# Kernel optimization log

Hardware: AMD Instinct MI355X
Metric: run time of the kernel (lower is better)

Reference implementation:

```python
import jax, jax.numpy as jnp
import numpy as np

BL = 5
N = 2 ** BL  # 32; LUT is (N+1) x (N+1)


def setup_inputs() -> dict:
    key = jax.random.key(0)
    k1, k2, k3 = jax.random.split(key, 3)
    M, K, O = 512, 256, 256
    x = jax.random.uniform(k1, (M, K), dtype=jnp.float32)              # activations in [0,1)
    W = jax.random.uniform(k2, (O, K), dtype=jnp.float32) * 2.0 - 1.0  # weights in [-1,1)
    b = jax.random.uniform(k3, (O,), dtype=jnp.float32) * 2.0 - 1.0
    # Stochastic-computing multiplication LUT: A[i, j] ~ i*j/N (floored), i,j in [0, N]
    i = np.arange(N + 1, dtype=np.float32)
    lut = jnp.asarray(np.floor(np.outer(i, i) / N), dtype=jnp.float32)
    return {"x": x, "W": W, "b": b, "lut": lut}


def _sanitize(t):
    t = jnp.where(jnp.isnan(t), jnp.zeros_like(t), t)
    return jnp.where(jnp.isinf(t), jnp.ones_like(t), t)


def sc_mat_mac_p(a, b, c, lut, n):
    # Faithful port of SC_MAT_MAC_p: quantize -> LUT gather over all (row, out) pairs ->
    # sign-correct -> reduce over K -> requantize -> add quantized bias -> rescale.
    a = _sanitize(a)
    b = _sanitize(b)
    c = _sanitize(c)
    amax = jnp.abs(a).max()
    amax = jnp.where(amax == 0, jnp.ones_like(amax), amax)
    dmax = jnp.maximum(jnp.abs(b).max(), jnp.abs(c).max())
    dmax = jnp.where(dmax == 0, jnp.ones_like(dmax), dmax)
    # SBL2 = int(log2(int(N / amax))); SN2 = 2**SBL2 (truncations match torch int())
    sn2 = 2.0 ** jnp.floor(jnp.log2(jnp.floor(n / amax)))
    sn1 = 2.0 ** jnp.floor(jnp.log2(jnp.floor(n / dmax)))
    aa = (a * sn2).astype(jnp.int32)  # [M, K], |aa| <= N
    bb = (b * sn1).astype(jnp.int32)  # [O, K], |bb| <= N
    cc = (c * sn1).astype(jnp.int32)  # [O]
    # LUT gather over the full cross product (original materializes this via
    # repeat_interleave/repeat; here it is a broadcasted gather of shape [M, O, K]).
    prod = lut[jnp.abs(aa)[:, None, :], jnp.abs(bb)[None, :, :]]          # [M, O, K]
    sgn = (jnp.sign(aa)[:, None, :] * jnp.sign(bb)[None, :, :]).astype(prod.dtype)
    x9 = (sgn * prod).sum(axis=-1)                                        # [M, O]
    d = (x9 / sn2).astype(jnp.int32) + cc[None, :]
    return d.astype(jnp.float32) / sn1


def reference(x, W, b, lut):
    # out = linear(x); out.data = SC_MAT_MAC_p(...)  -> value is the SC result,
    # gradient path is the dense linear (straight-through via .data assignment).
    lin = x @ W.T + b
    p = sc_mat_mac_p(x, W, b, lut, N)
    return lin + jax.lax.stop_gradient(p - lin)
```

## Files before the change

### kernel.cpp

```cpp
#include <hip/hip_runtime.h>
#include <stdint.h>


#define MROWS 512
#define KDIM  256
#define OCOLS 256
#define E2_GUESS 5
#define E1_GUESS 5

__device__ __forceinline__ void get_scales(float amax, float dmax, int& e2, int& e1) {
    if (amax == 0.0f) amax = 1.0f;
    if (dmax == 0.0f) dmax = 1.0f;
    float q2 = 32.0f / amax;
    float q1 = 32.0f / dmax;
    int f2 = (q2 >= 1073741824.0f) ? 0x40000000 : (int)floorf(q2);
    int f1 = (q1 >= 1073741824.0f) ? 0x40000000 : (int)floorf(q1);
    if (f2 < 1) f2 = 1;
    if (f1 < 1) f1 = 1;
    e2 = 31 - __clz(f2);
    e1 = 31 - __clz(f1);
}

__device__ __forceinline__ float max4(float4 v) {
    return fmaxf(fmaxf(fabsf(v.x), fabsf(v.y)), fmaxf(fabsf(v.z), fabsf(v.w)));
}

__device__ __forceinline__ void quant_row(const float* __restrict__ x, int m, int o,
                                          float sn2f, unsigned int* a_sh) {
    if (o < KDIM / 4) {
        float4 xv = ((const float4*)(x + (size_t)m * KDIM))[o];
        int a0 = (int)(xv.x * sn2f) & 0xFF;
        int a1 = (int)(xv.y * sn2f) & 0xFF;
        int a2 = (int)(xv.z * sn2f) & 0xFF;
        int a3 = (int)(xv.w * sn2f) & 0xFF;
        a_sh[o] = (unsigned int)(a0 | (a1 << 8) | (a2 << 16) | (a3 << 24));
    }
}

__device__ __forceinline__ int mac_loop(const float* __restrict__ W, int o,
                                        const unsigned int* a_sh, float sn1f) {
    const float4* wrow = (const float4*)(W + (size_t)o * KDIM);
    int sum = 0;
    #pragma unroll 8
    for (int kk = 0; kk < KDIM / 4; ++kk) {
        float4 wv = wrow[kk];
        unsigned int ap = a_sh[kk];
        float wfv[4] = {wv.x, wv.y, wv.z, wv.w};
        #pragma unroll
        for (int j = 0; j < 4; ++j) {
            int bv = (int)(wfv[j] * sn1f);
            int av = ((int)(ap << (24 - 8 * j))) >> 24;
            int s  = av * bv;
            sum += (s + ((s >> 31) & 31)) >> 5;
        }
    }
    return sum;
}

__global__ __launch_bounds__(256, 2)
void k_one(unsigned int* __restrict__ wsp, const float* __restrict__ x,
           const float* __restrict__ W, const float* __restrict__ b,
           float* __restrict__ out) {
    __shared__ unsigned int a_sh[KDIM / 4];
    __shared__ float sm[8];
    __shared__ int s_e[2];

    const int m = blockIdx.x;
    const int o = threadIdx.x;
    const int wave = o >> 6;

    if (m < 64) {
        const float4* xf = (const float4*)x;
        const float4* wf = (const float4*)W;
        float va = fmaxf(max4(xf[m * 512 + o]), max4(xf[m * 512 + 256 + o]));
        float vd = max4(wf[m * 256 + o]);
        if (m == 0 && o < 64)
            vd = fmaxf(vd, max4(((const float4*)b)[o]));
        #pragma unroll
        for (int s = 32; s >= 1; s >>= 1) {
            va = fmaxf(va, __shfl_xor(va, s, 64));
            vd = fmaxf(vd, __shfl_xor(vd, s, 64));
        }
        if ((o & 63) == 0) { sm[2 * wave] = va; sm[2 * wave + 1] = vd; }
        __syncthreads();
        if (o == 0) {
            float a = fmaxf(fmaxf(sm[0], sm[2]), fmaxf(sm[4], sm[6]));
            float d = fmaxf(fmaxf(sm[1], sm[3]), fmaxf(sm[5], sm[7]));
            __hip_atomic_store(&wsp[2 * m],     __float_as_uint(a),
                               __ATOMIC_RELAXED, __HIP_MEMORY_SCOPE_AGENT);
            __hip_atomic_store(&wsp[2 * m + 1], __float_as_uint(d),
                               __ATOMIC_RELAXED, __HIP_MEMORY_SCOPE_AGENT);
        }
        __syncthreads();
    }

    float bo = b[o];
    quant_row(x, m, o, (float)(1 << E2_GUESS), a_sh);
    __syncthreads();
    int sum = mac_loop(W, o, a_sh, (float)(1 << E1_GUESS));

    if (wave == 0) {
        unsigned int w0, w1;
        bool all;
        do {
            w0 = __hip_atomic_load(&wsp[2 * o],     __ATOMIC_RELAXED, __HIP_MEMORY_SCOPE_AGENT);
            w1 = __hip_atomic_load(&wsp[2 * o + 1], __ATOMIC_RELAXED, __HIP_MEMORY_SCOPE_AGENT);
            all = __all(((w0 | w1) & 0x80000000u) == 0u);
            if (!all) __builtin_amdgcn_s_sleep(1);
        } while (!all);
        float va = __uint_as_float(w0);
        float vd = __uint_as_float(w1);
        #pragma unroll
        for (int s = 32; s >= 1; s >>= 1) {
            va = fmaxf(va, __shfl_xor(va, s, 64));
            vd = fmaxf(vd, __shfl_xor(vd, s, 64));
        }
        if (o == 0) {
            int e2, e1;
            get_scales(va, vd, e2, e1);
            s_e[0] = e2; s_e[1] = e1;
        }
    }
    __syncthreads();

    const int e2 = s_e[0];
    const int e1 = s_e[1];

    if ((e2 != E2_GUESS) | (e1 != E1_GUESS)) {
        quant_row(x, m, o, (float)(1 << e2), a_sh);
        __syncthreads();
        sum = mac_loop(W, o, a_sh, (float)(1 << e1));
    }

    const float sn1f = (float)(1 << e1);
    int cc = (int)(bo * sn1f);
    int d  = ((sum + ((sum >> 31) & ((1 << e2) - 1))) >> e2) + cc;
    out[(size_t)m * OCOLS + o] = (float)d * (1.0f / sn1f);
}

extern "C" void kernel_launch(void* const* d_in, const int* in_sizes, int n_in,
                              void* d_out, int out_size, void* d_ws, size_t ws_size,
                              hipStream_t stream) {
    const float* x = (const float*)d_in[0];
    const float* W = (const float*)d_in[1];
    const float* b = (const float*)d_in[2];
    float* out = (float*)d_out;
    unsigned int* wsp = (unsigned int*)d_ws;

    k_one<<<MROWS, 256, 0, stream>>>(wsp, x, W, b, out);
}
```

Measured before the change: 74.99 us.

## Replace cross-block max handshake with per-block redundant max reduction

Removes the workspace-based inter-block spin wait used to share the global abs-max of x, W and b. Each block now scans all of x for its max and folds the W abs-max into the MAC loop that already streams all of W. This avoids the inter-block dependency and polling, but multiplies global/L2 reads of x by the number of blocks.

```diff
diff --git a/kernel.cpp b/kernel.cpp
--- a/kernel.cpp
+++ b/kernel.cpp
@@ -38,7 +38,31 @@
 }
 
 __device__ __forceinline__ int mac_loop(const float* __restrict__ W, int o,
-                                        const unsigned int* a_sh, float sn1f) {
+                                        const unsigned int* a_sh, float sn1f,
+                                        float& wmax) {
+    const float4* wrow = (const float4*)(W + (size_t)o * KDIM);
+    int sum = 0;
+    float wm = 0.0f;
+    #pragma unroll 8
+    for (int kk = 0; kk < KDIM / 4; ++kk) {
+        float4 wv = wrow[kk];
+        unsigned int ap = a_sh[kk];
+        float wfv[4] = {wv.x, wv.y, wv.z, wv.w};
+        #pragma unroll
+        for (int j = 0; j < 4; ++j) {
+            wm = fmaxf(wm, fabsf(wfv[j]));
+            int bv = (int)(wfv[j] * sn1f);
+            int av = ((int)(ap << (24 - 8 * j))) >> 24;
+            int s  = av * bv;
+            sum += (s + ((s >> 31) & 31)) >> 5;
+        }
+    }
+    wmax = wm;
+    return sum;
+}
+
+__device__ __forceinline__ int mac_loop_plain(const float* __restrict__ W, int o,
+                                              const unsigned int* a_sh, float sn1f) {
     const float4* wrow = (const float4*)(W + (size_t)o * KDIM);
     int sum = 0;
     #pragma unroll 8
@@ -58,78 +82,49 @@
 }
 
 __global__ __launch_bounds__(256, 2)
-void k_one(unsigned int* __restrict__ wsp, const float* __restrict__ x,
-           const float* __restrict__ W, const float* __restrict__ b,
-           float* __restrict__ out) {
+void k_one(const float* __restrict__ x, const float* __restrict__ W,
+           const float* __restrict__ b, float* __restrict__ out) {
     __shared__ unsigned int a_sh[KDIM / 4];
     __shared__ float sm[8];
-    __shared__ int s_e[2];
 
     const int m = blockIdx.x;
     const int o = threadIdx.x;
     const int wave = o >> 6;
 
-    if (m < 64) {
-        const float4* xf = (const float4*)x;
-        const float4* wf = (const float4*)W;
-        float va = fmaxf(max4(xf[m * 512 + o]), max4(xf[m * 512 + 256 + o]));
-        float vd = max4(wf[m * 256 + o]);
-        if (m == 0 && o < 64)
-            vd = fmaxf(vd, max4(((const float4*)b)[o]));
-        #pragma unroll
-        for (int s = 32; s >= 1; s >>= 1) {
-            va = fmaxf(va, __shfl_xor(va, s, 64));
-            vd = fmaxf(vd, __shfl_xor(vd, s, 64));
-        }
-        if ((o & 63) == 0) { sm[2 * wave] = va; sm[2 * wave + 1] = vd; }
-        __syncthreads();
-        if (o == 0) {
-            float a = fmaxf(fmaxf(sm[0], sm[2]), fmaxf(sm[4], sm[6]));
-            float d = fmaxf(fmaxf(sm[1], sm[3]), fmaxf(sm[5], sm[7]));
-            __hip_atomic_store(&wsp[2 * m],     __float_as_uint(a),
-                               __ATOMIC_RELAXED, __HIP_MEMORY_SCOPE_AGENT);
-            __hip_atomic_store(&wsp[2 * m + 1], __float_as_uint(d),
-                               __ATOMIC_RELAXED, __HIP_MEMORY_SCOPE_AGENT);
-        }
-        __syncthreads();
-    }
+    float bo = b[o];
 
-    float bo = b[o];
     quant_row(x, m, o, (float)(1 << E2_GUESS), a_sh);
     __syncthreads();
-    int sum = mac_loop(W, o, a_sh, (float)(1 << E1_GUESS));
+    float wmax;
+    int sum = mac_loop(W, o, a_sh, (float)(1 << E1_GUESS), wmax);
 
-    if (wave == 0) {
-        unsigned int w0, w1;
-        bool all;
-        do {
-            w0 = __hip_atomic_load(&wsp[2 * o],     __ATOMIC_RELAXED, __HIP_MEMORY_SCOPE_AGENT);
-            w1 = __hip_atomic_load(&wsp[2 * o + 1], __ATOMIC_RELAXED, __HIP_MEMORY_SCOPE_AGENT);
-            all = __all(((w0 | w1) & 0x80000000u) == 0u);
-            if (!all) __builtin_amdgcn_s_sleep(1);
-        } while (!all);
-        float va = __uint_as_float(w0);
-        float vd = __uint_as_float(w1);
-        #pragma unroll
-        for (int s = 32; s >= 1; s >>= 1) {
-            va = fmaxf(va, __shfl_xor(va, s, 64));
-            vd = fmaxf(vd, __shfl_xor(vd, s, 64));
-        }
-        if (o == 0) {
-            int e2, e1;
-            get_scales(va, vd, e2, e1);
-            s_e[0] = e2; s_e[1] = e1;
-        }
+    float xmax = 0.0f;
+    {
+        const float4* xf = (const float4*)x;
+        #pragma unroll 8
+        for (int i = 0; i < 128; ++i)
+            xmax = fmaxf(xmax, max4(xf[i * 256 + o]));
     }
+    float dmaxv = fmaxf(wmax, fabsf(bo));
+
+    #pragma unroll
+    for (int s = 32; s >= 1; s >>= 1) {
+        xmax  = fmaxf(xmax,  __shfl_xor(xmax,  s, 64));
+        dmaxv = fmaxf(dmaxv, __shfl_xor(dmaxv, s, 64));
+    }
+    if ((o & 63) == 0) { sm[2 * wave] = xmax; sm[2 * wave + 1] = dmaxv; }
     __syncthreads();
+    xmax  = fmaxf(fmaxf(sm[0], sm[2]), fmaxf(sm[4], sm[6]));
+    dmaxv = fmaxf(fmaxf(sm[1], sm[3]), fmaxf(sm[5], sm[7]));
 
-    const int e2 = s_e[0];
-    const int e1 = s_e[1];
+    int e2, e1;
+    get_scales(xmax, dmaxv, e2, e1);
 
     if ((e2 != E2_GUESS) | (e1 != E1_GUESS)) {
+        __syncthreads();
         quant_row(x, m, o, (float)(1 << e2), a_sh);
         __syncthreads();
-        sum = mac_loop(W, o, a_sh, (float)(1 << e1));
+        sum = mac_loop_plain(W, o, a_sh, (float)(1 << e1));
     }
 
     const float sn1f = (float)(1 << e1);
@@ -145,7 +140,6 @@
     const float* W = (const float*)d_in[1];
     const float* b = (const float*)d_in[2];
     float* out = (float*)d_out;
-    unsigned int* wsp = (unsigned int*)d_ws;
 
-    k_one<<<MROWS, 256, 0, stream>>>(wsp, x, W, b, out);
+    k_one<<<MROWS, 256, 0, stream>>>(x, W, b, out);
 }
```

Result: slower. 96.63 us (+28.9%).
